# Kernel optimization log

Measured on AMD Instinct MI355X. Metric: run time of the kernel, lower is better.

Reference implementation:

```python
import jax, jax.numpy as jnp
import numpy as np

N, H, V = 8192, 1024, 32000
IGNORE_INDEX = -100
LABEL_SMOOTHING = 0.0
LOGIT_SCALE = 1.0


def setup_inputs() -> dict:
    key = jax.random.key(0)
    k1, k2, k3 = jax.random.split(key, 3)
    x = jax.random.normal(k1, (N, H), dtype=jnp.float32)
    weight = jax.random.normal(k2, (V, H), dtype=jnp.float32) * 0.02
    bias = jnp.zeros((V,), dtype=jnp.float32)
    target = jax.random.randint(k3, (N,), 0, V, dtype=jnp.int64)
    return {"x": x, "weight": weight, "bias": bias, "target": target}


def reference(x, weight, bias, target):
    # logits: [N, V]; fused kernel never materializes this fully, but math is identical
    logits = (x @ weight.T + bias) * LOGIT_SCALE
    lse = jax.nn.logsumexp(logits.astype(jnp.float32), axis=-1)  # [N]
    valid = target != IGNORE_INDEX
    safe_t = jnp.where(valid, target, 0)
    tgt_logit = jnp.take_along_axis(logits, safe_t[:, None], axis=-1)[:, 0]
    loss_i = lse - tgt_logit
    if LABEL_SMOOTHING > 0:
        eps = LABEL_SMOOTHING / V
        z = (-eps * logits).sum(-1)
        loss_i = loss_i * (1.0 - LABEL_SMOOTHING) + (z + LABEL_SMOOTHING * lse)
    loss_i = jnp.where(valid, loss_i, 0.0)
    total = jnp.maximum(valid.sum(), 1)
    # reduction == 'mean': each per-token loss divided by total, then summed
    return loss_i.sum() / total
```

## Files before the change

kernel.cpp:

```cpp
#include <hip/hip_runtime.h>
#include <math.h>

typedef int    intx8    __attribute__((ext_vector_type(8)));
typedef float  floatx16 __attribute__((ext_vector_type(16)));

#define N_ROWS 8192
#define H_DIM  1024
#define V_DIM  32000
#define V_PAD  32768
#define IGNORE_INDEX (-100)

#define S_SPLITS 16
#define TILES_PER_SPLIT 16
#define BM 256
#define BN 128
#define BK 128

#define LOG2E 1.4426950408889634f
#define LN2   0.6931471805599453f

__global__ __launch_bounds__(256) void convert_fp8(const float* __restrict__ in,
                                                   unsigned char* __restrict__ out,
                                                   int Rstride, float scale) {
  const int r = blockIdx.x * 256 + threadIdx.x;
  const int u = blockIdx.y;
  const float4* src = (const float4*)(in + (size_t)r * H_DIM + u * 16);
  uint4 res;
#pragma unroll
  for (int j = 0; j < 4; ++j) {
    const float4 v = src[j];
    int p = __builtin_amdgcn_cvt_pk_fp8_f32(v.x * scale, v.y * scale, 0, false);
    p = __builtin_amdgcn_cvt_pk_fp8_f32(v.z * scale, v.w * scale, p, true);
    ((int*)&res)[j] = p;
  }
  *(uint4*)(out + ((size_t)u * Rstride + r) * 16) = res;
}

__global__ __launch_bounds__(256) void pad_bias(const float* __restrict__ bias,
                                                float* __restrict__ biasp) {
  const int i = blockIdx.x * 256 + threadIdx.x;
  biasp[i] = (i < V_DIM) ? bias[i] * LOG2E : -1e30f;
}

__global__ __launch_bounds__(256, 2) void flce_main(const unsigned char* __restrict__ xs,
                                                    const unsigned char* __restrict__ wsb,
                                                    const float* __restrict__ biasp,
                                                    float* __restrict__ partials) {
  __shared__ __align__(16) unsigned char smA[8 * 256 * 16];
  __shared__ __align__(16) unsigned char smB[8 * 128 * 16];

  const int tid  = threadIdx.x;
  const int lane = tid & 63;
  const int w    = tid >> 6;
  const int l31  = lane & 31;
  const int half = lane >> 5;
  const int wr   = w * 64;
  const int row0 = blockIdx.x * BM;
  const int sidx = blockIdx.y;

  float l_state[32];
#pragma unroll
  for (int i = 0; i < 32; ++i) l_state[i] = 0.f;

#pragma unroll 1
  for (int ct = 0; ct < TILES_PER_SPLIT; ++ct) {
    const int n0 = (sidx * TILES_PER_SPLIT + ct) * BN;
    floatx16 acc[2][4];
#pragma unroll
    for (int mb = 0; mb < 2; ++mb)
#pragma unroll
      for (int nb = 0; nb < 4; ++nb)
#pragma unroll
        for (int i = 0; i < 16; ++i) acc[mb][nb][i] = 0.f;

#pragma unroll 1
    for (int k0i = 0; k0i < H_DIM / BK; ++k0i) {
      const int ub = k0i * 8;
      __syncthreads();
#pragma unroll
      for (int j = 0; j < 8; ++j) {
        const int c = j * 4 + w;
        const int u = c >> 2;
        const int rb = c & 3;
        __builtin_amdgcn_global_load_lds(
            (const __attribute__((address_space(1))) void*)(xs + ((size_t)(ub + u) * N_ROWS + row0 + rb * 64 + lane) * 16),
            (__attribute__((address_space(3))) void*)(smA + ((u * 256 + rb * 64 + lane) * 16)),
            16, 0, 0);
      }
#pragma unroll
      for (int j = 0; j < 4; ++j) {
        const int c = j * 4 + w;
        const int u = c >> 1;
        const int rb = c & 1;
        __builtin_amdgcn_global_load_lds(
            (const __attribute__((address_space(1))) void*)(wsb + ((size_t)(ub + u) * V_PAD + n0 + rb * 64 + lane) * 16),
            (__attribute__((address_space(3))) void*)(smB + ((u * 128 + rb * 64 + lane) * 16)),
            16, 0, 0);
      }
      __syncthreads();

#pragma unroll
      for (int s2 = 0; s2 < 2; ++s2) {
        const int ua = s2 * 4 + half * 2;
        union { intx8 v; uint4 q[2]; } a[2], b[4];
#pragma unroll
        for (int mb = 0; mb < 2; ++mb) {
          a[mb].q[0] = *(const uint4*)(smA + ((ua * 256 + wr + mb * 32 + l31) * 16));
          a[mb].q[1] = *(const uint4*)(smA + (((ua + 1) * 256 + wr + mb * 32 + l31) * 16));
        }
#pragma unroll
        for (int nb = 0; nb < 4; ++nb) {
          b[nb].q[0] = *(const uint4*)(smB + ((ua * 128 + nb * 32 + l31) * 16));
          b[nb].q[1] = *(const uint4*)(smB + (((ua + 1) * 128 + nb * 32 + l31) * 16));
        }
#pragma unroll
        for (int mb = 0; mb < 2; ++mb)
#pragma unroll
          for (int nb = 0; nb < 4; ++nb)
            acc[mb][nb] = __builtin_amdgcn_mfma_scale_f32_32x32x64_f8f6f4(
                a[mb].v, b[nb].v, acc[mb][nb],
                0, 0,
                0, 0x7F7F7F7F,
                0, 0x7F7F7F7F);
      }
    }

    float bnb[4];
#pragma unroll
    for (int nb = 0; nb < 4; ++nb) bnb[nb] = biasp[n0 + nb * 32 + l31];
#pragma unroll
    for (int mb = 0; mb < 2; ++mb)
#pragma unroll
      for (int r = 0; r < 16; ++r) {
        float s = exp2f(acc[mb][0][r] + bnb[0]) + exp2f(acc[mb][1][r] + bnb[1])
                + exp2f(acc[mb][2][r] + bnb[2]) + exp2f(acc[mb][3][r] + bnb[3]);
        l_state[mb * 16 + r] += s;
      }
  }

#pragma unroll
  for (int s = 0; s < 32; ++s) {
    float v = l_state[s];
#pragma unroll
    for (int off = 1; off < 32; off <<= 1) v += __shfl_xor(v, off, 64);
    l_state[s] = v;
  }

  if (l31 == 0) {
#pragma unroll
    for (int s = 0; s < 32; ++s) {
      const int mb = s >> 4, r = s & 15;
      const int row = wr + mb * 32 + 4 * half + (r & 3) + 8 * (r >> 2);
      partials[(size_t)(row0 + row) * S_SPLITS + sidx] = l_state[s];
    }
  }
}

__global__ __launch_bounds__(256) void tgt_kernel(const float* __restrict__ x,
                                                  const float* __restrict__ wgt,
                                                  const float* __restrict__ bias,
                                                  const int* __restrict__ target,
                                                  float* __restrict__ tgt_logit) {
  const int r = blockIdx.x * 4 + (threadIdx.x >> 6);
  const int lane = threadIdx.x & 63;
  const int t = target[r];
  const int tt = (t == IGNORE_INDEX) ? 0 : t;
  const float4* xr = (const float4*)(x + (size_t)r * H_DIM);
  const float4* wr = (const float4*)(wgt + (size_t)tt * H_DIM);
  float acc = 0.f;
#pragma unroll
  for (int i = 0; i < 4; ++i) {
    const float4 a = xr[lane + i * 64];
    const float4 b = wr[lane + i * 64];
    acc += a.x * b.x + a.y * b.y + a.z * b.z + a.w * b.w;
  }
#pragma unroll
  for (int off = 32; off >= 1; off >>= 1) acc += __shfl_xor(acc, off, 64);
  if (lane == 0) tgt_logit[r] = acc + bias[tt];
}

__global__ __launch_bounds__(256) void loss_rows(const float* __restrict__ partials,
                                                 const float* __restrict__ tgt_logit,
                                                 const int* __restrict__ target,
                                                 float* __restrict__ bsums) {
  const int r = blockIdx.x * 256 + threadIdx.x;
  float l = 0.f;
#pragma unroll
  for (int s = 0; s < S_SPLITS; ++s) l += partials[(size_t)r * S_SPLITS + s];
  const float lse = LN2 * __log2f(l);
  const bool valid = (target[r] != IGNORE_INDEX);
  float loss = valid ? (lse - tgt_logit[r]) : 0.f;
  float cnt  = valid ? 1.f : 0.f;
  const int lane = threadIdx.x & 63;
  const int w = threadIdx.x >> 6;
#pragma unroll
  for (int off = 32; off >= 1; off >>= 1) {
    loss += __shfl_xor(loss, off, 64);
    cnt  += __shfl_xor(cnt, off, 64);
  }
  __shared__ float sl[4], sc[4];
  if (lane == 0) { sl[w] = loss; sc[w] = cnt; }
  __syncthreads();
  if (threadIdx.x == 0) {
    float S = 0.f, C = 0.f;
    for (int i = 0; i < 4; ++i) { S += sl[i]; C += sc[i]; }
    bsums[blockIdx.x] = S;
    bsums[32 + blockIdx.x] = C;
  }
}

__global__ void finalize(const float* __restrict__ bsums, float* __restrict__ out) {
  const int t = threadIdx.x;
  float s = (t < 32) ? bsums[t] : 0.f;
  float c = (t < 32) ? bsums[32 + t] : 0.f;
#pragma unroll
  for (int off = 32; off >= 1; off >>= 1) {
    s += __shfl_xor(s, off, 64);
    c += __shfl_xor(c, off, 64);
  }
  if (t == 0) out[0] = s / fmaxf(c, 1.f);
}

extern "C" void kernel_launch(void* const* d_in, const int* in_sizes, int n_in,
                              void* d_out, int out_size, void* d_ws, size_t ws_size,
                              hipStream_t stream) {
  const float* x    = (const float*)d_in[0];
  const float* wgt  = (const float*)d_in[1];
  const float* bias = (const float*)d_in[2];
  const int*   tgt  = (const int*)d_in[3];
  float* out = (float*)d_out;

  char* ws = (char*)d_ws;
  const size_t XS8 = (size_t)N_ROWS * H_DIM;
  const size_t WS8 = (size_t)V_PAD * H_DIM;
  const size_t BP  = (size_t)V_PAD * 4;
  const size_t PB  = (size_t)N_ROWS * S_SPLITS * 4;
  unsigned char* xs8 = (unsigned char*)ws;
  unsigned char* ws8 = (unsigned char*)(ws + XS8);
  float* biasp    = (float*)(ws + XS8 + WS8);
  float* partials = (float*)(ws + XS8 + WS8 + BP);
  float* tgt_lg   = (float*)(ws + XS8 + WS8 + BP + PB);
  float* bsums    = (float*)(ws + XS8 + WS8 + BP + PB + (size_t)N_ROWS * 4);

  convert_fp8<<<dim3(N_ROWS / 256, H_DIM / 16), 256, 0, stream>>>(x, xs8, N_ROWS, LOG2E);
  convert_fp8<<<dim3(V_DIM / 256, H_DIM / 16), 256, 0, stream>>>(wgt, ws8, V_PAD, 1.0f);
  pad_bias<<<V_PAD / 256, 256, 0, stream>>>(bias, biasp);
  tgt_kernel<<<N_ROWS / 4, 256, 0, stream>>>(x, wgt, bias, tgt, tgt_lg);
  flce_main<<<dim3(N_ROWS / BM, S_SPLITS), 256, 0, stream>>>(xs8, ws8, biasp, partials);
  loss_rows<<<N_ROWS / 256, 256, 0, stream>>>(partials, tgt_lg, tgt, bsums);
  finalize<<<1, 64, 0, stream>>>(bsums, out);
}
```

Baseline: 495.9 us.

## Double-buffer LDS tiles in main GEMM loop and merge prep kernels into one launch

The main kernel now streams half-depth K chunks into two alternating LDS buffers. The DMA for the next chunk is issued before computing the current one, so global loads overlap MFMA work and each step needs one barrier instead of two. The four preprocessing kernels (two fp8 conversions, bias padding, target logit) are merged into a single launch keyed on block index, which removes launch gaps. It also switches to the raw hardware exp2 builtin. The tradeoff is smaller K steps per barrier and more loop iterations with branching for the epilogue.

```diff
diff --git a/kernel.cpp b/kernel.cpp
--- a/kernel.cpp
+++ b/kernel.cpp
@@ -14,16 +14,14 @@
 #define TILES_PER_SPLIT 16
 #define BM 256
 #define BN 128
-#define BK 128
+#define BK 64
 
 #define LOG2E 1.4426950408889634f
 #define LN2   0.6931471805599453f
 
-__global__ __launch_bounds__(256) void convert_fp8(const float* __restrict__ in,
-                                                   unsigned char* __restrict__ out,
-                                                   int Rstride, float scale) {
-  const int r = blockIdx.x * 256 + threadIdx.x;
-  const int u = blockIdx.y;
+__device__ __forceinline__ void conv_one(const float* __restrict__ in,
+                                         unsigned char* __restrict__ out,
+                                         int r, int u, int Rstride, float scale) {
   const float4* src = (const float4*)(in + (size_t)r * H_DIM + u * 16);
   uint4 res;
 #pragma unroll
@@ -36,18 +34,50 @@
   *(uint4*)(out + ((size_t)u * Rstride + r) * 16) = res;
 }
 
-__global__ __launch_bounds__(256) void pad_bias(const float* __restrict__ bias,
-                                                float* __restrict__ biasp) {
-  const int i = blockIdx.x * 256 + threadIdx.x;
-  biasp[i] = (i < V_DIM) ? bias[i] * LOG2E : -1e30f;
+__global__ __launch_bounds__(256) void prep_all(const float* __restrict__ x,
+                                                const float* __restrict__ wgt,
+                                                const float* __restrict__ bias,
+                                                const int* __restrict__ target,
+                                                unsigned char* __restrict__ xs8,
+                                                unsigned char* __restrict__ ws8,
+                                                float* __restrict__ biasp,
+                                                float* __restrict__ tgt_logit) {
+  const int bid = blockIdx.x;
+  const int tid = threadIdx.x;
+  if (bid < 8000) {
+    conv_one(wgt, ws8, (bid % 125) * 256 + tid, bid / 125, V_PAD, 1.0f);
+  } else if (bid < 10048) {
+    const int b = bid - 8000;
+    conv_one(x, xs8, (b % 32) * 256 + tid, b / 32, N_ROWS, LOG2E);
+  } else if (bid < 10176) {
+    const int i = (bid - 10048) * 256 + tid;
+    biasp[i] = (i < V_DIM) ? bias[i] * LOG2E : -1e30f;
+  } else {
+    const int r = (bid - 10176) * 4 + (tid >> 6);
+    const int lane = tid & 63;
+    const int t = target[r];
+    const int tt = (t == IGNORE_INDEX) ? 0 : t;
+    const float4* xr = (const float4*)(x + (size_t)r * H_DIM);
+    const float4* wr = (const float4*)(wgt + (size_t)tt * H_DIM);
+    float acc = 0.f;
+#pragma unroll
+    for (int i = 0; i < 4; ++i) {
+      const float4 a = xr[lane + i * 64];
+      const float4 b = wr[lane + i * 64];
+      acc += a.x * b.x + a.y * b.y + a.z * b.z + a.w * b.w;
+    }
+#pragma unroll
+    for (int off = 32; off >= 1; off >>= 1) acc += __shfl_xor(acc, off, 64);
+    if (lane == 0) tgt_logit[r] = acc + bias[tt];
+  }
 }
 
 __global__ __launch_bounds__(256, 2) void flce_main(const unsigned char* __restrict__ xs,
                                                     const unsigned char* __restrict__ wsb,
                                                     const float* __restrict__ biasp,
                                                     float* __restrict__ partials) {
-  __shared__ __align__(16) unsigned char smA[8 * 256 * 16];
-  __shared__ __align__(16) unsigned char smB[8 * 128 * 16];
+  __shared__ __align__(16) unsigned char smA[2][4 * 256 * 16];
+  __shared__ __align__(16) unsigned char smB[2][4 * 128 * 16];
 
   const int tid  = threadIdx.x;
   const int lane = tid & 63;
@@ -62,80 +92,97 @@
 #pragma unroll
   for (int i = 0; i < 32; ++i) l_state[i] = 0.f;
 
+  floatx16 acc[2][4];
+#pragma unroll
+  for (int mb = 0; mb < 2; ++mb)
+#pragma unroll
+    for (int nb = 0; nb < 4; ++nb)
+#pragma unroll
+      for (int i = 0; i < 16; ++i) acc[mb][nb][i] = 0.f;
+
+  auto issue_dma = [&](int f, int p) {
+    const int ct = f >> 4;
+    const int k  = f & 15;
+    const int n0 = (sidx * TILES_PER_SPLIT + ct) * BN;
+    const int ub = k * 4;
+#pragma unroll
+    for (int j = 0; j < 4; ++j) {
+      const int c = j * 4 + w;
+      const int u = c >> 2;
+      const int rb = c & 3;
+      __builtin_amdgcn_global_load_lds(
+          (const __attribute__((address_space(1))) void*)(xs + ((size_t)(ub + u) * N_ROWS + row0 + rb * 64 + lane) * 16),
+          (__attribute__((address_space(3))) void*)(smA[p] + ((u * 256 + rb * 64 + lane) * 16)),
+          16, 0, 0);
+    }
+#pragma unroll
+    for (int j = 0; j < 2; ++j) {
+      const int c = j * 4 + w;
+      const int u = c >> 1;
+      const int rb = c & 1;
+      __builtin_amdgcn_global_load_lds(
+          (const __attribute__((address_space(1))) void*)(wsb + ((size_t)(ub + u) * V_PAD + n0 + rb * 64 + lane) * 16),
+          (__attribute__((address_space(3))) void*)(smB[p] + ((u * 128 + rb * 64 + lane) * 16)),
+          16, 0, 0);
+    }
+  };
+
+  issue_dma(0, 0);
+  __syncthreads();
+
+  float bnb[4];
+  const int ua = half * 2;
+
 #pragma unroll 1
-  for (int ct = 0; ct < TILES_PER_SPLIT; ++ct) {
-    const int n0 = (sidx * TILES_PER_SPLIT + ct) * BN;
-    floatx16 acc[2][4];
+  for (int f = 0; f < TILES_PER_SPLIT * 16; ++f) {
+    const int p = f & 1;
+    if (f + 1 < TILES_PER_SPLIT * 16) issue_dma(f + 1, p ^ 1);
+
+    if ((f & 15) == 0) {
+      const int n0 = (sidx * TILES_PER_SPLIT + (f >> 4)) * BN;
+#pragma unroll
+      for (int nb = 0; nb < 4; ++nb) bnb[nb] = biasp[n0 + nb * 32 + l31];
+    }
+
+    union { intx8 v; uint4 q[2]; } a[2], b[4];
+#pragma unroll
+    for (int mb = 0; mb < 2; ++mb) {
+      a[mb].q[0] = *(const uint4*)(smA[p] + ((ua * 256 + wr + mb * 32 + l31) * 16));
+      a[mb].q[1] = *(const uint4*)(smA[p] + (((ua + 1) * 256 + wr + mb * 32 + l31) * 16));
+    }
+#pragma unroll
+    for (int nb = 0; nb < 4; ++nb) {
+      b[nb].q[0] = *(const uint4*)(smB[p] + ((ua * 128 + nb * 32 + l31) * 16));
+      b[nb].q[1] = *(const uint4*)(smB[p] + (((ua + 1) * 128 + nb * 32 + l31) * 16));
+    }
 #pragma unroll
     for (int mb = 0; mb < 2; ++mb)
 #pragma unroll
       for (int nb = 0; nb < 4; ++nb)
-#pragma unroll
-        for (int i = 0; i < 16; ++i) acc[mb][nb][i] = 0.f;
-
-#pragma unroll 1
-    for (int k0i = 0; k0i < H_DIM / BK; ++k0i) {
-      const int ub = k0i * 8;
-      __syncthreads();
-#pragma unroll
-      for (int j = 0; j < 8; ++j) {
-        const int c = j * 4 + w;
-        const int u = c >> 2;
-        const int rb = c & 3;
-        __builtin_amdgcn_global_load_lds(
-            (const __attribute__((address_space(1))) void*)(xs + ((size_t)(ub + u) * N_ROWS + row0 + rb * 64 + lane) * 16),
-            (__attribute__((address_space(3))) void*)(smA + ((u * 256 + rb * 64 + lane) * 16)),
-            16, 0, 0);
-      }
-#pragma unroll
-      for (int j = 0; j < 4; ++j) {
-        const int c = j * 4 + w;
-        const int u = c >> 1;
-        const int rb = c & 1;
-        __builtin_amdgcn_global_load_lds(
-            (const __attribute__((address_space(1))) void*)(wsb + ((size_t)(ub + u) * V_PAD + n0 + rb * 64 + lane) * 16),
-            (__attribute__((address_space(3))) void*)(smB + ((u * 128 + rb * 64 + lane) * 16)),
-            16, 0, 0);
-      }
-      __syncthreads();
-
-#pragma unroll
-      for (int s2 = 0; s2 < 2; ++s2) {
-        const int ua = s2 * 4 + half * 2;
-        union { intx8 v; uint4 q[2]; } a[2], b[4];
-#pragma unroll
-        for (int mb = 0; mb < 2; ++mb) {
-          a[mb].q[0] = *(const uint4*)(smA + ((ua * 256 + wr + mb * 32 + l31) * 16));
-          a[mb].q[1] = *(const uint4*)(smA + (((ua + 1) * 256 + wr + mb * 32 + l31) * 16));
+        acc[mb][nb] = __builtin_amdgcn_mfma_scale_f32_32x32x64_f8f6f4(
+            a[mb].v, b[nb].v, acc[mb][nb],
+            0, 0,
+            0, 0x7F7F7F7F,
+            0, 0x7F7F7F7F);
+
+    if ((f & 15) == 15) {
+#pragma unroll
+      for (int mb = 0; mb < 2; ++mb)
+#pragma unroll
+        for (int r = 0; r < 16; ++r) {
+          l_state[mb * 16 + r] += __builtin_amdgcn_exp2f(acc[mb][0][r] + bnb[0])
+                                + __builtin_amdgcn_exp2f(acc[mb][1][r] + bnb[1])
+                                + __builtin_amdgcn_exp2f(acc[mb][2][r] + bnb[2])
+                                + __builtin_amdgcn_exp2f(acc[mb][3][r] + bnb[3]);
         }
 #pragma unroll
-        for (int nb = 0; nb < 4; ++nb) {
-          b[nb].q[0] = *(const uint4*)(smB + ((ua * 128 + nb * 32 + l31) * 16));
-          b[nb].q[1] = *(const uint4*)(smB + (((ua + 1) * 128 + nb * 32 + l31) * 16));
-        }
-#pragma unroll
-        for (int mb = 0; mb < 2; ++mb)
-#pragma unroll
-          for (int nb = 0; nb < 4; ++nb)
-            acc[mb][nb] = __builtin_amdgcn_mfma_scale_f32_32x32x64_f8f6f4(
-                a[mb].v, b[nb].v, acc[mb][nb],
-                0, 0,
-                0, 0x7F7F7F7F,
-                0, 0x7F7F7F7F);
-      }
-    }
-
-    float bnb[4];
-#pragma unroll
-    for (int nb = 0; nb < 4; ++nb) bnb[nb] = biasp[n0 + nb * 32 + l31];
-#pragma unroll
-    for (int mb = 0; mb < 2; ++mb)
-#pragma unroll
-      for (int r = 0; r < 16; ++r) {
-        float s = exp2f(acc[mb][0][r] + bnb[0]) + exp2f(acc[mb][1][r] + bnb[1])
-                + exp2f(acc[mb][2][r] + bnb[2]) + exp2f(acc[mb][3][r] + bnb[3]);
-        l_state[mb * 16 + r] += s;
-      }
+      for (int mb = 0; mb < 2; ++mb)
+#pragma unroll
+        for (int nb = 0; nb < 4; ++nb)
+#pragma unroll
+          for (int i = 0; i < 16; ++i) acc[mb][nb][i] = 0.f;
+    }
+    __syncthreads();
   }
 
 #pragma unroll
@@ -154,29 +201,6 @@
       partials[(size_t)(row0 + row) * S_SPLITS + sidx] = l_state[s];
     }
   }
-}
-
-__global__ __launch_bounds__(256) void tgt_kernel(const float* __restrict__ x,
-                                                  const float* __restrict__ wgt,
-                                                  const float* __restrict__ bias,
-                                                  const int* __restrict__ target,
-                                                  float* __restrict__ tgt_logit) {
-  const int r = blockIdx.x * 4 + (threadIdx.x >> 6);
-  const int lane = threadIdx.x & 63;
-  const int t = target[r];
-  const int tt = (t == IGNORE_INDEX) ? 0 : t;
-  const float4* xr = (const float4*)(x + (size_t)r * H_DIM);
-  const float4* wr = (const float4*)(wgt + (size_t)tt * H_DIM);
-  float acc = 0.f;
-#pragma unroll
-  for (int i = 0; i < 4; ++i) {
-    const float4 a = xr[lane + i * 64];
-    const float4 b = wr[lane + i * 64];
-    acc += a.x * b.x + a.y * b.y + a.z * b.z + a.w * b.w;
-  }
-#pragma unroll
-  for (int off = 32; off >= 1; off >>= 1) acc += __shfl_xor(acc, off, 64);
-  if (lane == 0) tgt_logit[r] = acc + bias[tt];
 }
 
 __global__ __launch_bounds__(256) void loss_rows(const float* __restrict__ partials,
@@ -242,10 +266,7 @@
   float* tgt_lg   = (float*)(ws + XS8 + WS8 + BP + PB);
   float* bsums    = (float*)(ws + XS8 + WS8 + BP + PB + (size_t)N_ROWS * 4);
 
-  convert_fp8<<<dim3(N_ROWS / 256, H_DIM / 16), 256, 0, stream>>>(x, xs8, N_ROWS, LOG2E);
-  convert_fp8<<<dim3(V_DIM / 256, H_DIM / 16), 256, 0, stream>>>(wgt, ws8, V_PAD, 1.0f);
-  pad_bias<<<V_PAD / 256, 256, 0, stream>>>(bias, biasp);
-  tgt_kernel<<<N_ROWS / 4, 256, 0, stream>>>(x, wgt, bias, tgt, tgt_lg);
+  prep_all<<<12224, 256, 0, stream>>>(x, wgt, bias, tgt, xs8, ws8, biasp, tgt_lg);
   flce_main<<<dim3(N_ROWS / BM, S_SPLITS), 256, 0, stream>>>(xs8, ws8, biasp, partials);
   loss_rows<<<N_ROWS / 256, 256, 0, stream>>>(partials, tgt_lg, tgt, bsums);
   finalize<<<1, 64, 0, stream>>>(bsums, out);
```

Measured after the change: 498.3 us. Within noise of the previous version (+0.5%).
